# Optimization experiments

Hardware: AMD Instinct MI355X
Metric: run time of the kernel (lower is better)

Reference implementation:

```python
import jax, jax.numpy as jnp
import numpy as np

B = 8; NPB = 12500; N = B * NPB; DEG = 16; E = N * DEG
W_IMG, H_IMG = 240.0, 180.0
GX, GY = 15, 15
NC = GX * GY             # 225 clusters per sample
N2 = B * NC              # pooled node count (fixed)
CH = [1, 8, 8, 32, 32, 128]
NUM_OUT = 101
EPS = 1e-5


def _coarse_edges():
    # deterministic 8-neighborhood on the 15x15 pooled grid (torus), per sample
    gy, gx = np.meshgrid(np.arange(GY), np.arange(GX), indexing='ij')
    base = (gy * GX + gx).reshape(-1)
    srcs, dsts = [], []
    for dy in (-1, 0, 1):
        for dx in (-1, 0, 1):
            if dy == 0 and dx == 0:
                continue
            nb = (((gy + dy) % GY) * GX + (gx + dx) % GX).reshape(-1)
            srcs.append(nb); dsts.append(base)
    s = np.concatenate(srcs); d = np.concatenate(dsts)
    s = (s[None] + NC * np.arange(B)[:, None]).reshape(-1)
    d = (d[None] + NC * np.arange(B)[:, None]).reshape(-1)
    return np.stack([s, d]).astype(np.int32)


def setup_inputs():
    key = jax.random.key(0)
    ks = jax.random.split(key, 32)
    pos = jnp.concatenate([
        jax.random.uniform(ks[0], (N, 1)) * W_IMG,
        jax.random.uniform(ks[1], (N, 1)) * H_IMG,
        jax.random.uniform(ks[2], (N, 1))], axis=1)
    x = jax.random.normal(ks[3], (N, 1))
    batch = jnp.repeat(jnp.arange(B, dtype=jnp.int32), NPB)
    src = jax.random.randint(ks[4], (E,), 0, NPB, dtype=jnp.int32) + jnp.repeat(batch * NPB, DEG)
    dst = jnp.repeat(jnp.arange(N, dtype=jnp.int32), DEG)
    inp = {'x': x, 'pos': pos, 'batch': batch,
           'edge_index': jnp.stack([src, dst]),
           'edge_index2': jnp.asarray(_coarse_edges())}
    ki = 5
    for l in range(5):
        cin, cout = CH[l], CH[l + 1]
        for nm, fan in (('w_lin', cin), ('w_src', cin), ('w_dst', cin), ('w_pos', 3)):
            inp[f'{nm}{l+1}'] = jax.random.normal(ks[ki], (fan, cout)) / np.sqrt(fan)
            ki += 1
        inp[f'b_pos{l+1}'] = jnp.zeros((cout,))
        inp[f'g{l+1}'] = jnp.ones((cout,))
        inp[f'be{l+1}'] = jnp.zeros((cout,))
    inp['w_fc'] = jax.random.normal(ks[ki], (CH[5] * 16, NUM_OUT)) * 0.02
    return inp


def pt_conv(x, pos, src, dst, n_nodes, w_lin, w_src, w_dst, w_pos, b_pos):
    # PyG PointTransformerConv with add_self_loops=True, sum aggregation
    loops = jnp.arange(n_nodes, dtype=src.dtype)
    src = jnp.concatenate([src, loops]); dst = jnp.concatenate([dst, loops])
    h = x @ w_lin                           # value transform [N, cout]
    a_src = x @ w_src; a_dst = x @ w_dst
    delta = (pos[dst] - pos[src]) @ w_pos + b_pos      # pos_nn(pos_i - pos_j)
    alpha = a_dst[dst] - a_src[src] + delta            # [E, cout]
    amax = jax.ops.segment_max(alpha, dst, num_segments=n_nodes)
    amax = jnp.where(jnp.isneginf(amax), 0.0, amax)
    ex = jnp.exp(alpha - amax[dst])
    denom = jax.ops.segment_sum(ex, dst, num_segments=n_nodes)
    attn = ex / (denom[dst] + 1e-16)
    msg = attn * (h[src] + delta)
    return jax.ops.segment_sum(msg, dst, num_segments=n_nodes)


def bn(x, g, b):
    mu = x.mean(0)
    var = x.var(0)
    return g * (x - mu) * jax.lax.rsqrt(var + EPS) + b


def pool3(x, pos, batch):
    # voxel-grid max pool (16,12), fixed N2 clusters; pos -> cluster mean
    cx = jnp.clip(jnp.floor(pos[:, 0] / 16.0).astype(jnp.int32), 0, GX - 1)
    cy = jnp.clip(jnp.floor(pos[:, 1] / 12.0).astype(jnp.int32), 0, GY - 1)
    cl = batch * NC + cy * GX + cx
    x2 = jax.ops.segment_max(x, cl, num_segments=N2)
    x2 = jnp.where(jnp.isneginf(x2), 0.0, x2)
    cnt = jax.ops.segment_sum(jnp.ones((pos.shape[0], 1), pos.dtype), cl, num_segments=N2)
    pos2 = jax.ops.segment_sum(pos, cl, num_segments=N2) / jnp.maximum(cnt, 1.0)
    return x2, pos2


def pool5(x2, pos2):
    # MaxPoolingX: 4x4 grid (cell size 60x45), 16 clusters per sample
    batch2 = jnp.arange(N2, dtype=jnp.int32) // NC
    cx = jnp.clip(jnp.floor(pos2[:, 0] / (W_IMG / 4)).astype(jnp.int32), 0, 3)
    cy = jnp.clip(jnp.floor(pos2[:, 1] / (H_IMG / 4)).astype(jnp.int32), 0, 3)
    cl = batch2 * 16 + cy * 4 + cx
    out = jax.ops.segment_max(x2, cl, num_segments=B * 16)
    out = jnp.where(jnp.isneginf(out), 0.0, out)
    return out.reshape(B, 16 * CH[5])


def _forward(x, pos, batch, edge_index, edge_index2, convs, bns, w_fc):
    src, dst = edge_index[0], edge_index[1]
    h = bn(jax.nn.elu(pt_conv(x, pos, src, dst, N, *convs[0])), *bns[0])
    sc = h
    h = bn(jax.nn.elu(pt_conv(h, pos, src, dst, N, *convs[1])), *bns[1]) + sc
    h = bn(jax.nn.elu(pt_conv(h, pos, src, dst, N, *convs[2])), *bns[2])
    h2, pos2 = pool3(h, pos, batch)
    s2, d2 = edge_index2[0], edge_index2[1]
    sc = h2
    h2 = bn(jax.nn.elu(pt_conv(h2, pos2, s2, d2, N2, *convs[3])), *bns[3]) + sc
    h2 = bn(jax.nn.elu(pt_conv(h2, pos2, s2, d2, N2, *convs[4])), *bns[4])
    return pool5(h2, pos2) @ w_fc


def reference(x, pos, batch, edge_index, edge_index2,
              w_lin1, w_src1, w_dst1, w_pos1, b_pos1, g1, be1,
              w_lin2, w_src2, w_dst2, w_pos2, b_pos2, g2, be2,
              w_lin3, w_src3, w_dst3, w_pos3, b_pos3, g3, be3,
              w_lin4, w_src4, w_dst4, w_pos4, b_pos4, g4, be4,
              w_lin5, w_src5, w_dst5, w_pos5, b_pos5, g5, be5,
              w_fc):
    convs = [(w_lin1, w_src1, w_dst1, w_pos1, b_pos1),
             (w_lin2, w_src2, w_dst2, w_pos2, b_pos2),
             (w_lin3, w_src3, w_dst3, w_pos3, b_pos3),
             (w_lin4, w_src4, w_dst4, w_pos4, b_pos4),
             (w_lin5, w_src5, w_dst5, w_pos5, b_pos5)]
    bns = [(g1, be1), (g2, be2), (g3, be3), (g4, be4), (g5, be5)]
    return _forward(x, pos, batch, edge_index, edge_index2, convs, bns, w_fc)
```

## Files before the change

kernel.cpp:

```cpp
#include <hip/hip_runtime.h>

#define ENC_NEGINF 0x007FFFFFu
#define NN_FINE 100000
#define NN_COARSE 1800
#define INV_N  (1.0f / 100000.0f)
#define INV_N2 (1.0f / 1800.0f)

__device__ __forceinline__ unsigned enc_f(float f) {
    unsigned u = __float_as_uint(f);
    return (u & 0x80000000u) ? ~u : (u | 0x80000000u);
}
__device__ __forceinline__ float dec_f(unsigned k) {
    return (k & 0x80000000u) ? __uint_as_float(k & 0x7fffffffu) : __uint_as_float(~k);
}

__device__ __forceinline__ int xcd_swz(int bid, int nwg) {
    int q = nwg >> 3, r = nwg & 7;
    int xcd = bid & 7, idx = bid >> 3;
    return (xcd < r ? xcd * (q + 1) : r * (q + 1) + (xcd - r) * q) + idx;
}

__device__ __forceinline__ float2 bn_ss(const float* __restrict__ st,
                                        const float* __restrict__ g,
                                        const float* __restrict__ be,
                                        int r, float invn) {
    float mu  = st[r] * invn;
    float var = fmaxf(st[128 + r] * invn - mu * mu, 0.f);
    float s = g[r] * rsqrtf(var + 1e-5f);
    return make_float2(s, be[r] - mu * s);
}

__global__ void init_k(float* stats, float* out) {
    int t = blockIdx.x * blockDim.x + threadIdx.x;
    if (t < 1280) stats[t] = 0.f;
    if (t < 808)  out[t] = 0.f;
}

template<int CIN, int COUT, int MODE>
__global__ void pass_a(const float* __restrict__ in,
                       const float* __restrict__ st, const float* __restrict__ g,
                       const float* __restrict__ be, float invn,
                       const float* __restrict__ skipf,
                       const float* __restrict__ wl, const float* __restrict__ wsrc,
                       const float* __restrict__ wpos, const float* __restrict__ bpos,
                       const float* __restrict__ pos,
                       float4* __restrict__ SHP, float2* __restrict__ CAP,
                       float* __restrict__ zout, int NN) {
    constexpr int P = COUT / 2;
    int idx = blockIdx.x * blockDim.x + threadIdx.x;
    int i = idx / P, p = idx % P;
    if (i >= NN) return;
    float f[CIN];
#pragma unroll
    for (int r = 0; r < CIN; ++r) {
        float v = in[i * CIN + r];
        if constexpr (MODE >= 1) {
            float2 ss = bn_ss(st, g, be, r, invn);
            v = v * ss.x + ss.y;
        }
        if constexpr (MODE == 2) v += skipf[i * CIN + r];
        f[r] = v;
    }
    int c0 = 2 * p;
    float h0 = 0.f, a0 = 0.f, h1 = 0.f, a1 = 0.f;
#pragma unroll
    for (int r = 0; r < CIN; ++r) {
        float2 wlr = *reinterpret_cast<const float2*>(&wl[r * COUT + c0]);
        float2 wsr = *reinterpret_cast<const float2*>(&wsrc[r * COUT + c0]);
        h0 += f[r] * wlr.x; h1 += f[r] * wlr.y;
        a0 += f[r] * wsr.x; a1 += f[r] * wsr.y;
    }
    float px = pos[i * 3], py = pos[i * 3 + 1], pz = pos[i * 3 + 2];
    float2 w0 = *reinterpret_cast<const float2*>(&wpos[c0]);
    float2 w1 = *reinterpret_cast<const float2*>(&wpos[COUT + c0]);
    float2 w2 = *reinterpret_cast<const float2*>(&wpos[2 * COUT + c0]);
    float pd0 = px * w0.x + py * w1.x + pz * w2.x;
    float pd1 = px * w0.y + py * w1.y + pz * w2.y;
    float2 bp = *reinterpret_cast<const float2*>(&bpos[c0]);
    SHP[(size_t)i * P + p] = make_float4(a0 + pd0, a1 + pd1, h0 - pd0, h1 - pd1);
    CAP[(size_t)i * P + p] = make_float2(pd0 + bp.x, pd1 + bp.y);
    if constexpr (MODE == 1) {
        float2 s0 = bn_ss(st, g, be, c0, invn);
        float2 s1 = bn_ss(st, g, be, c0 + 1, invn);
        float2 zv = make_float2(in[i * CIN + c0] * s0.x + s0.y,
                                in[i * CIN + c0 + 1] * s1.x + s1.y);
        *reinterpret_cast<float2*>(&zout[i * CIN + c0]) = zv;
    }
}

template<int C, bool COARSE>
__global__ __launch_bounds__(256, 4)
void edge_pass(const float4* __restrict__ SHP, const float2* __restrict__ CAP,
               const int* __restrict__ esrc, float2* __restrict__ y2,
               float* __restrict__ PS, int NN) {
    constexpr int P = C / 2;
    constexpr int NPB = 256 / P;
    constexpr int DEG_ = COARSE ? 8 : 16;
    __shared__ int se[NPB * DEG_];
    __shared__ float ls[C], lq[C];
    int bid = COARSE ? (int)blockIdx.x : xcd_swz(blockIdx.x, gridDim.x);
    int tid = threadIdx.x;
    int node0 = bid * NPB;
    if constexpr (!COARSE) {
        for (int t = tid; t < NPB * DEG_; t += 256)
            se[t] = esrc[node0 * 16 + t];
    } else {
        for (int t = tid; t < NPB * DEG_; t += 256) {
            int n = t / DEG_, e = t % DEG_;
            int i2 = node0 + n;
            if (i2 < NN) {
                int b = i2 / 225, j = i2 % 225;
                se[t] = esrc[b * 1800 + e * 225 + j];
            }
        }
    }
    if (tid < C) { ls[tid] = 0.f; lq[tid] = 0.f; }
    __syncthreads();
    int n = tid / P, p = tid % P;
    int i = node0 + n;
    float y0 = 0.f, y1 = 0.f;
    if (i < NN) {
        float4 q[DEG_ + 1];
#pragma unroll
        for (int e = 0; e < DEG_; ++e)
            q[e] = SHP[(size_t)se[n * DEG_ + e] * P + p];
        q[DEG_] = SHP[(size_t)i * P + p];

        float smin0 = q[0].x, smin1 = q[0].y;
#pragma unroll
        for (int e = 1; e <= DEG_; ++e) {
            smin0 = fminf(smin0, q[e].x);
            smin1 = fminf(smin1, q[e].y);
        }
        float den0 = 0.f, acc0 = 0.f, den1 = 0.f, acc1 = 0.f;
#pragma unroll
        for (int e = 0; e <= DEG_; ++e) {
            float ex0 = __expf(smin0 - q[e].x);
            float ex1 = __expf(smin1 - q[e].y);
            den0 += ex0; acc0 += ex0 * q[e].z;
            den1 += ex1; acc1 += ex1 * q[e].w;
        }
        float2 Ci = CAP[(size_t)i * P + p];
        float o0 = (acc0 + Ci.x * den0) / (den0 + 1e-16f);
        float o1 = (acc1 + Ci.y * den1) / (den1 + 1e-16f);
        y0 = o0 > 0.f ? o0 : (__expf(o0) - 1.f);
        y1 = o1 > 0.f ? o1 : (__expf(o1) - 1.f);
        y2[(size_t)i * P + p] = make_float2(y0, y1);
    }
    float sa0 = y0, sq0 = y0 * y0, sa1 = y1, sq1 = y1 * y1;
    if constexpr (P < 64) {
#pragma unroll
        for (int m = P; m < 64; m <<= 1) {
            sa0 += __shfl_xor(sa0, m); sa1 += __shfl_xor(sa1, m);
            sq0 += __shfl_xor(sq0, m); sq1 += __shfl_xor(sq1, m);
        }
    }
    if ((tid & 63) < P) {
        int c0 = 2 * p;
        atomicAdd(&ls[c0], sa0); atomicAdd(&ls[c0 + 1], sa1);
        atomicAdd(&lq[c0], sq0); atomicAdd(&lq[c0 + 1], sq1);
    }
    __syncthreads();
    if (tid < C) {
        PS[(size_t)blockIdx.x * 2 * C + tid]     = ls[tid];
        PS[(size_t)blockIdx.x * 2 * C + C + tid] = lq[tid];
    }
}

template<int C>
__global__ __launch_bounds__(256)
void stats_r(const float* __restrict__ PS, int nb, float* __restrict__ STATS) {
    constexpr int TC = 2 * C;
    constexpr int NS = 256 / TC;
    __shared__ float acc[256];
    int tid = threadIdx.x;
    int c = tid % TC, sl = tid / TC;
    float s = 0.f;
    for (int b = blockIdx.x * NS + sl; b < nb; b += gridDim.x * NS)
        s += PS[(size_t)b * TC + c];
    acc[tid] = s;
    __syncthreads();
    if (tid < TC) {
        float t = 0.f;
#pragma unroll
        for (int s2 = 0; s2 < NS; ++s2) t += acc[s2 * TC + tid];
        float* dst = (tid < C) ? &STATS[tid] : &STATS[128 + (tid - C)];
        atomicAdd(dst, t);
    }
}

__global__ __launch_bounds__(256)
void pool3a(const float* __restrict__ y3, const float* __restrict__ st,
            const float* __restrict__ g, const float* __restrict__ be,
            const float* __restrict__ pos,
            unsigned* __restrict__ PK, float* __restrict__ PC,
            float* __restrict__ PP) {
    __shared__ unsigned lkey[7200];
    __shared__ float lcnt[225];
    __shared__ float lpac[675];
    int tid = threadIdx.x;
    for (int t = tid; t < 7200; t += 256) lkey[t] = ENC_NEGINF;
    if (tid < 225) lcnt[tid] = 0.f;
    for (int t = tid; t < 675; t += 256) lpac[t] = 0.f;
    __syncthreads();
    int bid = blockIdx.x;
    int s = bid >> 5, sb = bid & 31;
    int beg = s * 12500 + sb * 391;
    int end = min(s * 12500 + 12500, beg + 391);
    int c = tid & 31, nl = tid >> 5;
    float2 ss = bn_ss(st, g, be, c, INV_N);
    for (int i = beg + nl; i < end; i += 8) {
        float z = y3[(size_t)i * 32 + c] * ss.x + ss.y;
        float px = pos[i * 3], py = pos[i * 3 + 1];
        int cx = min(max((int)floorf(px / 16.f), 0), 14);
        int cy = min(max((int)floorf(py / 12.f), 0), 14);
        int cl = cy * 15 + cx;
        atomicMax(&lkey[cl * 32 + c], enc_f(z));
        if (c == 0) {
            atomicAdd(&lcnt[cl], 1.f);
            atomicAdd(&lpac[cl * 3 + 0], px);
            atomicAdd(&lpac[cl * 3 + 1], py);
            atomicAdd(&lpac[cl * 3 + 2], pos[i * 3 + 2]);
        }
    }
    __syncthreads();
    for (int t = tid; t < 7200; t += 256) PK[(size_t)bid * 7200 + t] = lkey[t];
    if (tid < 225) PC[bid * 225 + tid] = lcnt[tid];
    for (int t = tid; t < 675; t += 256) PP[bid * 675 + t] = lpac[t];
}

__global__ void pool3b(const unsigned* __restrict__ PK, const float* __restrict__ PC,
                       const float* __restrict__ PP,
                       float* __restrict__ X2, float* __restrict__ POS2) {
    int idx = blockIdx.x * blockDim.x + threadIdx.x;
    if (idx < 57600) {
        int s = idx / 7200, t = idx % 7200;
        unsigned m = ENC_NEGINF;
#pragma unroll 8
        for (int sb = 0; sb < 32; ++sb)
            m = max(m, PK[(size_t)(s * 32 + sb) * 7200 + t]);
        X2[idx] = (m == ENC_NEGINF) ? 0.f : dec_f(m);
    } else if (idx < 63000) {
        int j = idx - 57600;
        int s = j / 675, r = j % 675;
        int cl = r / 3;
        float sp = 0.f, sc = 0.f;
#pragma unroll 8
        for (int sb = 0; sb < 32; ++sb) {
            sp += PP[(s * 32 + sb) * 675 + r];
            sc += PC[(s * 32 + sb) * 225 + cl];
        }
        POS2[j] = sp / fmaxf(sc, 1.f);
    }
}

__global__ __launch_bounds__(1024)
void pool5_k(const float* __restrict__ y5, const float* __restrict__ st,
             const float* __restrict__ g, const float* __restrict__ be,
             const float* __restrict__ POS2, float* __restrict__ POOLED) {
    __shared__ unsigned lkey[2048];
    int tid = threadIdx.x, s = blockIdx.x;
    for (int t = tid; t < 2048; t += 1024) lkey[t] = ENC_NEGINF;
    __syncthreads();
    int c = tid & 127, nl = tid >> 7;
    float2 ss = bn_ss(st, g, be, c, INV_N2);
    for (int j = nl; j < 225; j += 8) {
        int i = s * 225 + j;
        float z = y5[(size_t)i * 128 + c] * ss.x + ss.y;
        float px = POS2[i * 3], py = POS2[i * 3 + 1];
        int cx = min(max((int)floorf(px / 60.f), 0), 3);
        int cy = min(max((int)floorf(py / 45.f), 0), 3);
        atomicMax(&lkey[(cy * 4 + cx) * 128 + c], enc_f(z));
    }
    __syncthreads();
    for (int t = tid; t < 2048; t += 1024) {
        unsigned k = lkey[t];
        POOLED[s * 2048 + t] = (k == ENC_NEGINF) ? 0.f : dec_f(k);
    }
}

__global__ __launch_bounds__(256)
void fc_k(const float* __restrict__ POOLED, const float* __restrict__ wfc,
          float* __restrict__ out) {
    __shared__ float row[128];
    __shared__ float acc[256];
    int s = blockIdx.x, kc = blockIdx.y;
    int k0 = kc * 128;
    int tid = threadIdx.x;
    if (tid < 128) row[tid] = POOLED[s * 2048 + k0 + tid];
    __syncthreads();
    int o = tid & 127, half = tid >> 7;
    float a = 0.f;
    if (o < 101) {
        int kk0 = half * 64;
        for (int kk = kk0; kk < kk0 + 64; ++kk)
            a += row[kk] * wfc[(size_t)(k0 + kk) * 101 + o];
    }
    acc[tid] = a;
    __syncthreads();
    if (tid < 128 && o < 101)
        atomicAdd(&out[s * 101 + o], acc[tid] + acc[tid + 128]);
}

extern "C" void kernel_launch(void* const* d_in, const int* in_sizes, int n_in,
                              void* d_out, int out_size, void* d_ws, size_t ws_size,
                              hipStream_t stream) {
    const float* x     = (const float*)d_in[0];
    const float* pos   = (const float*)d_in[1];
    const int*   e1    = (const int*)d_in[3];
    const int*   e2    = (const int*)d_in[4];
    const float* w_fc  = (const float*)d_in[40];
    auto WL = [&](int l) { return (const float*)d_in[5 + l * 7 + 0]; };
    auto WS = [&](int l) { return (const float*)d_in[5 + l * 7 + 1]; };
    auto WP = [&](int l) { return (const float*)d_in[5 + l * 7 + 3]; };
    auto BP = [&](int l) { return (const float*)d_in[5 + l * 7 + 4]; };
    auto G_ = [&](int l) { return (const float*)d_in[5 + l * 7 + 5]; };
    auto BE = [&](int l) { return (const float*)d_in[5 + l * 7 + 6]; };

    float* W = (float*)d_ws;
    size_t o = 0;
    float4* SHPf = (float4*)W;        o += 6400000;
    float2* CAPf = (float2*)(W + o);  o += 3200000;
    float*  Y1   = W + o;             o += 800000;
    float*  Y2   = W + o;             o += 800000;
    float*  Z1   = W + o;             o += 800000;
    float*  Y3   = W + o;             o += 3200000;
    float*  STATS = W + o;            o += 5 * 256;
    float*  X2   = W + o;             o += 57600;
    float*  POS2 = W + o;             o += 5400;
    float4* SHPc = (float4*)(W + o);  o += 460800;
    float2* CAPc = (float2*)(W + o);  o += 230400;
    float*  Y4   = W + o;             o += 57600;
    float*  Y5   = W + o;             o += 230400;
    float*  POOLED = W + o;           o += 16384;
    float*  PSTAT  = W + o;           o += 400000;
    unsigned* PK = (unsigned*)W;
    float*    PC = W + 2000000;
    float*    PP = W + 2100000;

    hipLaunchKernelGGL(init_k, dim3(2), dim3(1024), 0, stream, STATS, (float*)d_out);

    hipLaunchKernelGGL((pass_a<1, 8, 0>), dim3(1563), dim3(256), 0, stream,
                       x, nullptr, nullptr, nullptr, 0.f, nullptr,
                       WL(0), WS(0), WP(0), BP(0), pos,
                       SHPf, CAPf, nullptr, NN_FINE);
    hipLaunchKernelGGL((edge_pass<8, false>), dim3(1563), dim3(256), 0, stream,
                       SHPf, CAPf, e1, (float2*)Y1, PSTAT, NN_FINE);
    hipLaunchKernelGGL((stats_r<8>), dim3(32), dim3(256), 0, stream,
                       PSTAT, 1563, STATS + 0);

    hipLaunchKernelGGL((pass_a<8, 8, 1>), dim3(1563), dim3(256), 0, stream,
                       Y1, STATS + 0, G_(0), BE(0), INV_N, nullptr,
                       WL(1), WS(1), WP(1), BP(1), pos,
                       SHPf, CAPf, Z1, NN_FINE);
    hipLaunchKernelGGL((edge_pass<8, false>), dim3(1563), dim3(256), 0, stream,
                       SHPf, CAPf, e1, (float2*)Y2, PSTAT, NN_FINE);
    hipLaunchKernelGGL((stats_r<8>), dim3(32), dim3(256), 0, stream,
                       PSTAT, 1563, STATS + 256);

    hipLaunchKernelGGL((pass_a<8, 32, 2>), dim3(6250), dim3(256), 0, stream,
                       Y2, STATS + 256, G_(1), BE(1), INV_N, Z1,
                       WL(2), WS(2), WP(2), BP(2), pos,
                       SHPf, CAPf, nullptr, NN_FINE);
    hipLaunchKernelGGL((edge_pass<32, false>), dim3(6250), dim3(256), 0, stream,
                       SHPf, CAPf, e1, (float2*)Y3, PSTAT, NN_FINE);
    hipLaunchKernelGGL((stats_r<32>), dim3(32), dim3(256), 0, stream,
                       PSTAT, 6250, STATS + 512);

    hipLaunchKernelGGL(pool3a, dim3(256), dim3(256), 0, stream,
                       Y3, STATS + 512, G_(2), BE(2), pos, PK, PC, PP);
    hipLaunchKernelGGL(pool3b, dim3(247), dim3(256), 0, stream,
                       PK, PC, PP, X2, POS2);

    hipLaunchKernelGGL((pass_a<32, 32, 0>), dim3(113), dim3(256), 0, stream,
                       X2, nullptr, nullptr, nullptr, 0.f, nullptr,
                       WL(3), WS(3), WP(3), BP(3), POS2,
                       SHPc, CAPc, nullptr, NN_COARSE);
    hipLaunchKernelGGL((edge_pass<32, true>), dim3(113), dim3(256), 0, stream,
                       SHPc, CAPc, e2, (float2*)Y4, PSTAT, NN_COARSE);
    hipLaunchKernelGGL((stats_r<32>), dim3(16), dim3(256), 0, stream,
                       PSTAT, 113, STATS + 768);

    hipLaunchKernelGGL((pass_a<32, 128, 2>), dim3(450), dim3(256), 0, stream,
                       Y4, STATS + 768, G_(3), BE(3), INV_N2, X2,
                       WL(4), WS(4), WP(4), BP(4), POS2,
                       SHPc, CAPc, nullptr, NN_COARSE);
    hipLaunchKernelGGL((edge_pass<128, true>), dim3(450), dim3(256), 0, stream,
                       SHPc, CAPc, e2, (float2*)Y5, PSTAT, NN_COARSE);
    hipLaunchKernelGGL((stats_r<128>), dim3(16), dim3(256), 0, stream,
                       PSTAT, 450, STATS + 1024);

    hipLaunchKernelGGL(pool5_k, dim3(8), dim3(1024), 0, stream,
                       Y5, STATS + 1024, G_(4), BE(4), POS2, POOLED);
    hipLaunchKernelGGL(fc_k, dim3(8, 16), dim3(256), 0, stream,
                       POOLED, w_fc, (float*)d_out);
}
```

Baseline: 228.1 us.

## Fold init into first pass, defer pool3 batch-norm, double pool3 partitions

The separate init kernel is removed: the first pass_a launch now zeroes the stats and output buffers, saving one launch. pool3a no longer applies the layer-3 batch-norm per element. It takes the max of the raw values, and pool3b applies the scale and shift once per pooled output, reading the stats there. pool3a also splits each sample into 64 sub-blocks instead of 32 for more parallelism, at the cost of a larger partial buffer and a longer reduction in pool3b. Applying the norm after the max is only equivalent when the norm scale is positive, which holds for unit gamma but not for arbitrary gamma.

```diff
diff --git a/kernel.cpp b/kernel.cpp
--- a/kernel.cpp
+++ b/kernel.cpp
@@ -28,12 +28,6 @@
     float var = fmaxf(st[128 + r] * invn - mu * mu, 0.f);
     float s = g[r] * rsqrtf(var + 1e-5f);
     return make_float2(s, be[r] - mu * s);
-}
-
-__global__ void init_k(float* stats, float* out) {
-    int t = blockIdx.x * blockDim.x + threadIdx.x;
-    if (t < 1280) stats[t] = 0.f;
-    if (t < 808)  out[t] = 0.f;
 }
 
 template<int CIN, int COUT, int MODE>
@@ -45,11 +39,16 @@
                        const float* __restrict__ wpos, const float* __restrict__ bpos,
                        const float* __restrict__ pos,
                        float4* __restrict__ SHP, float2* __restrict__ CAP,
-                       float* __restrict__ zout, int NN) {
+                       float* __restrict__ zout, int total,
+                       float* __restrict__ zstats, float* __restrict__ zo) {
     constexpr int P = COUT / 2;
     int idx = blockIdx.x * blockDim.x + threadIdx.x;
+    if (zstats) {
+        if (idx < 1280) zstats[idx] = 0.f;
+        if (idx < 808)  zo[idx] = 0.f;
+    }
+    if (idx >= total) return;
     int i = idx / P, p = idx % P;
-    if (i >= NN) return;
     float f[CIN];
 #pragma unroll
     for (int r = 0; r < CIN; ++r) {
@@ -190,9 +189,7 @@
 }
 
 __global__ __launch_bounds__(256)
-void pool3a(const float* __restrict__ y3, const float* __restrict__ st,
-            const float* __restrict__ g, const float* __restrict__ be,
-            const float* __restrict__ pos,
+void pool3a(const float* __restrict__ y3, const float* __restrict__ pos,
             unsigned* __restrict__ PK, float* __restrict__ PC,
             float* __restrict__ PP) {
     __shared__ unsigned lkey[7200];
@@ -204,13 +201,12 @@
     for (int t = tid; t < 675; t += 256) lpac[t] = 0.f;
     __syncthreads();
     int bid = blockIdx.x;
-    int s = bid >> 5, sb = bid & 31;
-    int beg = s * 12500 + sb * 391;
-    int end = min(s * 12500 + 12500, beg + 391);
+    int s = bid >> 6, sb = bid & 63;
+    int beg = s * 12500 + sb * 196;
+    int end = min(s * 12500 + 12500, beg + 196);
     int c = tid & 31, nl = tid >> 5;
-    float2 ss = bn_ss(st, g, be, c, INV_N);
     for (int i = beg + nl; i < end; i += 8) {
-        float z = y3[(size_t)i * 32 + c] * ss.x + ss.y;
+        float z = y3[(size_t)i * 32 + c];
         float px = pos[i * 3], py = pos[i * 3 + 1];
         int cx = min(max((int)floorf(px / 16.f), 0), 14);
         int cy = min(max((int)floorf(py / 12.f), 0), 14);
@@ -230,25 +226,27 @@
 }
 
 __global__ void pool3b(const unsigned* __restrict__ PK, const float* __restrict__ PC,
-                       const float* __restrict__ PP,
+                       const float* __restrict__ PP, const float* __restrict__ ST3,
+                       const float* __restrict__ g3, const float* __restrict__ be3,
                        float* __restrict__ X2, float* __restrict__ POS2) {
     int idx = blockIdx.x * blockDim.x + threadIdx.x;
     if (idx < 57600) {
         int s = idx / 7200, t = idx % 7200;
         unsigned m = ENC_NEGINF;
 #pragma unroll 8
-        for (int sb = 0; sb < 32; ++sb)
-            m = max(m, PK[(size_t)(s * 32 + sb) * 7200 + t]);
-        X2[idx] = (m == ENC_NEGINF) ? 0.f : dec_f(m);
+        for (int sb = 0; sb < 64; ++sb)
+            m = max(m, PK[(size_t)(s * 64 + sb) * 7200 + t]);
+        float2 ss = bn_ss(ST3, g3, be3, t & 31, INV_N);
+        X2[idx] = (m == ENC_NEGINF) ? 0.f : (dec_f(m) * ss.x + ss.y);
     } else if (idx < 63000) {
         int j = idx - 57600;
         int s = j / 675, r = j % 675;
         int cl = r / 3;
         float sp = 0.f, sc = 0.f;
 #pragma unroll 8
-        for (int sb = 0; sb < 32; ++sb) {
-            sp += PP[(s * 32 + sb) * 675 + r];
-            sc += PC[(s * 32 + sb) * 225 + cl];
+        for (int sb = 0; sb < 64; ++sb) {
+            sp += PP[(s * 64 + sb) * 675 + r];
+            sc += PC[(s * 64 + sb) * 225 + cl];
         }
         POS2[j] = sp / fmaxf(sc, 1.f);
     }
@@ -310,12 +308,7 @@
     const int*   e1    = (const int*)d_in[3];
     const int*   e2    = (const int*)d_in[4];
     const float* w_fc  = (const float*)d_in[40];
-    auto WL = [&](int l) { return (const float*)d_in[5 + l * 7 + 0]; };
-    auto WS = [&](int l) { return (const float*)d_in[5 + l * 7 + 1]; };
-    auto WP = [&](int l) { return (const float*)d_in[5 + l * 7 + 3]; };
-    auto BP = [&](int l) { return (const float*)d_in[5 + l * 7 + 4]; };
-    auto G_ = [&](int l) { return (const float*)d_in[5 + l * 7 + 5]; };
-    auto BE = [&](int l) { return (const float*)d_in[5 + l * 7 + 6]; };
+    auto F = [&](int idx) { return (const float*)d_in[idx]; };
 
     float* W = (float*)d_ws;
     size_t o = 0;
@@ -335,63 +328,61 @@
     float*  POOLED = W + o;           o += 16384;
     float*  PSTAT  = W + o;           o += 400000;
     unsigned* PK = (unsigned*)W;
-    float*    PC = W + 2000000;
-    float*    PP = W + 2100000;
-
-    hipLaunchKernelGGL(init_k, dim3(2), dim3(1024), 0, stream, STATS, (float*)d_out);
+    float*    PC = W + 5600000;
+    float*    PP = W + 5800000;
 
     hipLaunchKernelGGL((pass_a<1, 8, 0>), dim3(1563), dim3(256), 0, stream,
                        x, nullptr, nullptr, nullptr, 0.f, nullptr,
-                       WL(0), WS(0), WP(0), BP(0), pos,
-                       SHPf, CAPf, nullptr, NN_FINE);
+                       F(5), F(6), F(8), F(9), pos, SHPf, CAPf, nullptr, 400000,
+                       STATS, (float*)d_out);
     hipLaunchKernelGGL((edge_pass<8, false>), dim3(1563), dim3(256), 0, stream,
                        SHPf, CAPf, e1, (float2*)Y1, PSTAT, NN_FINE);
     hipLaunchKernelGGL((stats_r<8>), dim3(32), dim3(256), 0, stream,
                        PSTAT, 1563, STATS + 0);
 
     hipLaunchKernelGGL((pass_a<8, 8, 1>), dim3(1563), dim3(256), 0, stream,
-                       Y1, STATS + 0, G_(0), BE(0), INV_N, nullptr,
-                       WL(1), WS(1), WP(1), BP(1), pos,
-                       SHPf, CAPf, Z1, NN_FINE);
+                       Y1, STATS + 0, F(10), F(11), INV_N, nullptr,
+                       F(12), F(13), F(15), F(16), pos, SHPf, CAPf, Z1, 400000,
+                       nullptr, nullptr);
     hipLaunchKernelGGL((edge_pass<8, false>), dim3(1563), dim3(256), 0, stream,
                        SHPf, CAPf, e1, (float2*)Y2, PSTAT, NN_FINE);
     hipLaunchKernelGGL((stats_r<8>), dim3(32), dim3(256), 0, stream,
                        PSTAT, 1563, STATS + 256);
 
     hipLaunchKernelGGL((pass_a<8, 32, 2>), dim3(6250), dim3(256), 0, stream,
-                       Y2, STATS + 256, G_(1), BE(1), INV_N, Z1,
-                       WL(2), WS(2), WP(2), BP(2), pos,
-                       SHPf, CAPf, nullptr, NN_FINE);
+                       Y2, STATS + 256, F(17), F(18), INV_N, Z1,
+                       F(19), F(20), F(22), F(23), pos, SHPf, CAPf, nullptr, 1600000,
+                       nullptr, nullptr);
     hipLaunchKernelGGL((edge_pass<32, false>), dim3(6250), dim3(256), 0, stream,
                        SHPf, CAPf, e1, (float2*)Y3, PSTAT, NN_FINE);
     hipLaunchKernelGGL((stats_r<32>), dim3(32), dim3(256), 0, stream,
                        PSTAT, 6250, STATS + 512);
 
-    hipLaunchKernelGGL(pool3a, dim3(256), dim3(256), 0, stream,
-                       Y3, STATS + 512, G_(2), BE(2), pos, PK, PC, PP);
+    hipLaunchKernelGGL(pool3a, dim3(512), dim3(256), 0, stream,
+                       Y3, pos, PK, PC, PP);
     hipLaunchKernelGGL(pool3b, dim3(247), dim3(256), 0, stream,
-                       PK, PC, PP, X2, POS2);
+                       PK, PC, PP, STATS + 512, F(24), F(25), X2, POS2);
 
     hipLaunchKernelGGL((pass_a<32, 32, 0>), dim3(113), dim3(256), 0, stream,
                        X2, nullptr, nullptr, nullptr, 0.f, nullptr,
-                       WL(3), WS(3), WP(3), BP(3), POS2,
-                       SHPc, CAPc, nullptr, NN_COARSE);
+                       F(26), F(27), F(29), F(30), POS2, SHPc, CAPc, nullptr, 28800,
+                       nullptr, nullptr);
     hipLaunchKernelGGL((edge_pass<32, true>), dim3(113), dim3(256), 0, stream,
                        SHPc, CAPc, e2, (float2*)Y4, PSTAT, NN_COARSE);
     hipLaunchKernelGGL((stats_r<32>), dim3(16), dim3(256), 0, stream,
                        PSTAT, 113, STATS + 768);
 
     hipLaunchKernelGGL((pass_a<32, 128, 2>), dim3(450), dim3(256), 0, stream,
-                       Y4, STATS + 768, G_(3), BE(3), INV_N2, X2,
-                       WL(4), WS(4), WP(4), BP(4), POS2,
-                       SHPc, CAPc, nullptr, NN_COARSE);
+                       Y4, STATS + 768, F(31), F(32), INV_N2, X2,
+                       F(33), F(34), F(36), F(37), POS2, SHPc, CAPc, nullptr, 115200,
+                       nullptr, nullptr);
     hipLaunchKernelGGL((edge_pass<128, true>), dim3(450), dim3(256), 0, stream,
                        SHPc, CAPc, e2, (float2*)Y5, PSTAT, NN_COARSE);
     hipLaunchKernelGGL((stats_r<128>), dim3(16), dim3(256), 0, stream,
                        PSTAT, 450, STATS + 1024);
 
     hipLaunchKernelGGL(pool5_k, dim3(8), dim3(1024), 0, stream,
-                       Y5, STATS + 1024, G_(4), BE(4), POS2, POOLED);
+                       Y5, STATS + 1024, F(38), F(39), POS2, POOLED);
     hipLaunchKernelGGL(fc_k, dim3(8, 16), dim3(256), 0, stream,
                        POOLED, w_fc, (float*)d_out);
 }
```

After: 214.0 us, median of 2. 1.07x faster.
